# Performance work log

Hardware: AMD Instinct MI355X
Metric: run time of the kernel (lower is better)

## Reference

```python
import jax, jax.numpy as jnp
import numpy as np
from jax import lax

B, N, K, NUM_CLASS = 8, 4096, 16, 13


def knn(pc, k):
    # pc: (B, C, N); returns indices of k nearest neighbors (B, N, k)
    sq = jnp.sum(pc * pc, axis=1)                       # (B, N)
    inner = jnp.einsum('bcn,bcm->bnm', pc, pc)          # (B, N, N)
    neg_dist = 2.0 * inner - sq[:, :, None] - sq[:, None, :]
    return lax.top_k(neg_dist, k)[1]                    # (B, N, k)


def group(fea, idx):
    # fea: (B, C, N), idx: (B, N, k) -> (B, C, N, k)
    return jax.vmap(lambda f, i: f[:, i])(fea, idx)


def mlp2(x, w, b, act=True):
    # 1x1 conv2d: x (B, Cin, N, k) -> (B, Cout, N, k)
    y = jnp.einsum('oc,bcnk->bonk', w, x) + b[None, :, None, None]
    return jax.nn.relu(y) if act else y


def mlp1(x, w, b, act=True):
    # 1x1 conv1d: x (B, Cin, N) -> (B, Cout, N)
    y = jnp.einsum('oc,bcn->bon', w, x) + b[None, :, None]
    return jax.nn.relu(y) if act else y


def edgeconv(xyz, fea, k, wg1, bg1, wg2, bg2, wf1, bf1, wf2, bf2, wf3, bf3):
    idx = knn(fea, k)
    # geometric branch: (B, 10, N, k) = [dist, xyz, xyz_knn, xyz - xyz_knn]
    xk = group(xyz, idx)
    xc = jnp.broadcast_to(xyz[:, :, :, None], xk.shape)
    xr = xc - xk
    xd = jnp.sqrt(jnp.sum(xr * xr, axis=1, keepdims=True))
    g = jnp.concatenate([xd, xc, xk, xr], axis=1)
    # feature branch: (B, 2C, N, k) = [fea, fea_knn]
    fk = group(fea, idx)
    fc = jnp.broadcast_to(fea[:, :, :, None], fk.shape)
    f = jnp.concatenate([fc, fk], axis=1)
    g = mlp2(mlp2(g, wg1, bg1), wg2, bg2)
    f = mlp2(mlp2(mlp2(f, wf1, bf1), wf2, bf2), wf3, bf3)
    return jnp.max(g * f, axis=-1)  # (B, Cout, N)


_SPECS = [
    ('e1_mg1', 10, 32), ('e1_mg2', 32, 32),
    ('e1_mf1', 6, 32), ('e1_mf2', 32, 32), ('e1_mf3', 32, 32),
    ('e2_mg1', 10, 128), ('e2_mg2', 128, 128),
    ('e2_mf1', 64, 128), ('e2_mf2', 128, 128), ('e2_mf3', 128, 128),
    ('c1', 128, 128), ('c2', 128, 1024), ('c3', 1184, 512),
    ('c4', 512, 256), ('c5', 256, 128), ('c6', 128, NUM_CLASS),
]


def setup_inputs() -> dict:
    key = jax.random.key(0)
    ks = jax.random.split(key, 2 * len(_SPECS) + 1)
    inp = {'xyz': jax.random.normal(ks[0], (B, N, 3), dtype=jnp.float32)}
    for j, (name, ci, co) in enumerate(_SPECS):
        scale = 1.0 / np.sqrt(ci)
        inp['w_' + name] = jax.random.normal(ks[2 * j + 1], (co, ci), dtype=jnp.float32) * scale
        inp['b_' + name] = jax.random.normal(ks[2 * j + 2], (co,), dtype=jnp.float32) * 0.01
    return inp


def reference(xyz, w_e1_mg1, b_e1_mg1, w_e1_mg2, b_e1_mg2, w_e1_mf1, b_e1_mf1,
              w_e1_mf2, b_e1_mf2, w_e1_mf3, b_e1_mf3, w_e2_mg1, b_e2_mg1,
              w_e2_mg2, b_e2_mg2, w_e2_mf1, b_e2_mf1, w_e2_mf2, b_e2_mf2,
              w_e2_mf3, b_e2_mf3, w_c1, b_c1, w_c2, b_c2, w_c3, b_c3,
              w_c4, b_c4, w_c5, b_c5, w_c6, b_c6):
    x = jnp.transpose(xyz, (0, 2, 1))  # (B, 3, N)
    fea1 = edgeconv(x, x, K, w_e1_mg1, b_e1_mg1, w_e1_mg2, b_e1_mg2,
                    w_e1_mf1, b_e1_mf1, w_e1_mf2, b_e1_mf2, w_e1_mf3, b_e1_mf3)
    fea2 = edgeconv(x, fea1, K, w_e2_mg1, b_e2_mg1, w_e2_mg2, b_e2_mg2,
                    w_e2_mf1, b_e2_mf1, w_e2_mf2, b_e2_mf2, w_e2_mf3, b_e2_mf3)
    f = mlp1(fea2, w_c1, b_c1)
    f = mlp1(f, w_c2, b_c2)                        # (B, 1024, N)
    g = jnp.max(f, axis=-1, keepdims=True)         # global feature (B, 1024, 1)
    g = jnp.broadcast_to(g, (g.shape[0], g.shape[1], x.shape[2]))
    f = jnp.concatenate([fea1, fea2, g], axis=1)   # (B, 1184, N)
    f = mlp1(f, w_c3, b_c3)
    f = mlp1(f, w_c4, b_c4)
    f = mlp1(f, w_c5, b_c5)
    return mlp1(f, w_c6, b_c6, act=False)          # (B, NUM_CLASS, N)
```

## Files before the change

### kernel.cpp

```cpp
#include <hip/hip_runtime.h>
#include <math.h>

#define B_ 8
#define N_ 4096
#define PL_ (8 * 4096 * 32)

__device__ __forceinline__ unsigned short bf16rne(float x) {
    unsigned int u = __float_as_uint(x);
    return (unsigned short)((u + 0x7FFFu + ((u >> 16) & 1u)) >> 16);
}
__device__ __forceinline__ float bff(unsigned short h) {
    return __uint_as_float((unsigned int)h << 16);
}
__device__ __forceinline__ void cvt_hl(unsigned short* base, int numel, int idx, float x) {
    unsigned short h = bf16rne(x);
    base[idx] = h;
    base[numel + idx] = bf16rne(x - bff(h));
}

typedef __attribute__((ext_vector_type(8))) short bf16x8;
typedef __attribute__((ext_vector_type(4))) float f32x4;

#define MF16(a, b, c) __builtin_amdgcn_mfma_f32_16x16x32_bf16((a), (b), (c), 0, 0, 0)

__global__ __launch_bounds__(256) void prep_kernel(
    const float* __restrict__ w0, const float* __restrict__ w1,
    const float* __restrict__ w2, const float* __restrict__ w3,
    const float* __restrict__ w4, const float* __restrict__ w5,
    const float* __restrict__ w6, const float* __restrict__ w8,
    const float* __restrict__ w9, const float* __restrict__ w10,
    const float* __restrict__ w11, const float* __restrict__ w12,
    const float* __restrict__ w13, const float* __restrict__ w14,
    const float* __restrict__ wf1, const float* __restrict__ bf1,
    const float* __restrict__ xyz,
    float* __restrict__ wt, float* __restrict__ gbuf, float* __restrict__ sqbuf,
    unsigned short* __restrict__ xyzp) {
    const int g = blockIdx.x * 256 + threadIdx.x;
    unsigned short* wus = (unsigned short*)(wt + 3840);

    if (g < 3584) {
        if (g < 320)       { int i = g >> 5, o = g & 31;             wt[g] = w0[o * 10 + i]; }
        else if (g < 1344) { int l = g - 320;  int i = l >> 5, o = l & 31; wt[g] = w1[o * 32 + i]; }
        else if (g < 1536) { int l = g - 1344; int i = l >> 5, o = l & 31; wt[g] = w2[o * 6 + i]; }
        else if (g < 2560) { int l = g - 1536; int i = l >> 5, o = l & 31; wt[g] = w3[o * 32 + i]; }
        else               { int l = g - 2560; int i = l >> 5, o = l & 31; wt[g] = w4[o * 32 + i]; }
    }
    else if (g < 3840)   { int l = g - 3584; wt[g] = (l < 128) ? bf1[l] : 0.0f; }
    else if (g < 12032)  { int l = g - 3840; int o = l >> 5, i = l & 31;
                           float x = (o < 128) ? wf1[o * 64 + i] : wf1[(o - 128) * 64 + 32 + i];
                           cvt_hl(wus + 0, 8192, l, x); }
    else if (g < 28416)  { int l = g - 12032;  cvt_hl(wus + 16384, 16384, l, w10[l]); }
    else if (g < 159488) { int l = g - 28416;  cvt_hl(wus + 49152, 131072, l, w11[l]); }
    else if (g < 241408) { int l = g - 159488; int o = l / 160, i = l - o * 160;
                           cvt_hl(wus + 311296, 81920, l, w12[o * 1184 + i]); }
    else if (g < 372480) { int l = g - 241408; cvt_hl(wus + 475136, 131072, l, w13[l]); }
    else if (g < 405248) { int l = g - 372480; cvt_hl(wus + 737280, 32768, l, w14[l]); }
    else if (g < 409344) { int l = g - 405248; int o = l >> 5, k = l & 31;
                           float x = (k < 10) ? w5[o * 10 + k] : 0.0f;
                           cvt_hl(wus + 802816, 4096, l, x); }
    else if (g < 425728) { int l = g - 409344; cvt_hl(wus + 811008, 16384, l, w6[l]); }
    else if (g < 442112) { int l = g - 425728; cvt_hl(wus + 843776, 16384, l, w8[l]); }
    else if (g < 458496) { int l = g - 442112; cvt_hl(wus + 876544, 16384, l, w9[l]); }
    else if (g < 466688) { gbuf[g - 458496] = 0.0f; }
    else if (g < 499456) { int l = g - 466688;
                           const float* p = xyz + (size_t)l * 3;
                           sqbuf[l] = fmaf(p[0], p[0], fmaf(p[1], p[1], p[2] * p[2])); }
    else if (g < 532224) {
        int row = g - 499456;
        const float* p = xyz + (size_t)row * 3;
        unsigned short hv[8] = {0,0,0,0,0,0,0,0};
        unsigned short mv[8] = {0,0,0,0,0,0,0,0};
        unsigned short lv[8] = {0,0,0,0,0,0,0,0};
        #pragma unroll
        for (int c = 0; c < 3; ++c) {
            float v = p[c];
            unsigned short h = bf16rne(v); float d = v - bff(h);
            unsigned short m = bf16rne(d);
            hv[c] = h; mv[c] = m; lv[c] = bf16rne(d - bff(m));
        }
        uint4 z = make_uint4(0u, 0u, 0u, 0u);
        unsigned short* d0 = xyzp + (size_t)row * 32;
        unsigned short* d1 = d0 + PL_;
        unsigned short* d2 = d0 + 2 * PL_;
        *(uint4*)d0 = *(uint4*)hv; *(uint4*)(d0 + 8) = z; *(uint4*)(d0 + 16) = z; *(uint4*)(d0 + 24) = z;
        *(uint4*)d1 = *(uint4*)mv; *(uint4*)(d1 + 8) = z; *(uint4*)(d1 + 16) = z; *(uint4*)(d1 + 24) = z;
        *(uint4*)d2 = *(uint4*)lv; *(uint4*)(d2 + 8) = z; *(uint4*)(d2 + 16) = z; *(uint4*)(d2 + 24) = z;
    }
}

__global__ __launch_bounds__(256) void fea1p_kernel(
    const float* __restrict__ F, unsigned short* __restrict__ P, float* __restrict__ SQ) {
    int row = blockIdx.x * 256 + threadIdx.x;
    const float* x = F + (size_t)row * 32;
    float s = 0.0f;
    unsigned short hb[32], mb[32], lb[32];
    #pragma unroll
    for (int c = 0; c < 32; ++c) {
        float v = x[c];
        s = fmaf(v, v, s);
        unsigned short h = bf16rne(v); float d = v - bff(h);
        unsigned short m = bf16rne(d);
        hb[c] = h; mb[c] = m; lb[c] = bf16rne(d - bff(m));
    }
    SQ[row] = s;
    unsigned short* d0 = P + (size_t)row * 32;
    #pragma unroll
    for (int q = 0; q < 4; ++q) {
        *(uint4*)(d0 + 8 * q)           = *(uint4*)&hb[8 * q];
        *(uint4*)(d0 + PL_ + 8 * q)     = *(uint4*)&mb[8 * q];
        *(uint4*)(d0 + 2 * PL_ + 8 * q) = *(uint4*)&lb[8 * q];
    }
}


__device__ __forceinline__ void cas_asc(unsigned long long& x, unsigned long long& y) {
    unsigned long long a = x, b = y;
    bool sw = a > b;
    x = sw ? b : a;
    y = sw ? a : b;
}

__device__ __forceinline__ void merge_top(unsigned long long (&k)[16],
                                          const unsigned long long (&o)[16]) {
    #pragma unroll
    for (int i = 0; i < 16; ++i) {
        unsigned long long bb = o[15 - i];
        if (bb > k[i]) k[i] = bb;
    }
    #pragma unroll
    for (int st = 8; st >= 1; st >>= 1)
        #pragma unroll
        for (int i = 0; i < 16; ++i)
            if ((i & st) == 0) cas_asc(k[i], k[i + st]);
}

__device__ __forceinline__ void casv(float& x, float& y) {
    float lo = fminf(x, y), hi = fmaxf(x, y);
    x = lo; y = hi;
}

__device__ __forceinline__ void sortv16(float (&v)[16]) {
    #pragma unroll
    for (int sz = 2; sz <= 16; sz <<= 1)
        #pragma unroll
        for (int st = sz >> 1; st >= 1; st >>= 1)
            #pragma unroll
            for (int i = 0; i < 16; ++i)
                if ((i & st) == 0) {
                    if ((i & sz) == 0) casv(v[i], v[i + st]);
                    else                casv(v[i + st], v[i]);
                }
}

__device__ __forceinline__ void mergev(float (&kv)[16], const float (&nv)[16]) {
    #pragma unroll
    for (int i = 0; i < 16; ++i) kv[i] = fmaxf(kv[i], nv[15 - i]);
    #pragma unroll
    for (int st = 8; st >= 1; st >>= 1)
        #pragma unroll
        for (int i = 0; i < 16; ++i)
            if ((i & st) == 0) casv(kv[i], kv[i + st]);
}

__global__ __launch_bounds__(256, 4) void knn_kernel(
    const unsigned short* __restrict__ P, const float* __restrict__ SQ,
    unsigned long long* __restrict__ Kout) {
    __shared__ __align__(16) char U[64 * 68 * 4];
    __shared__ float sqcL[2048];
    __shared__ float tau[64];
    __shared__ int cnt[64];
    float* Ds = (float*)U;
    unsigned long long* cap = (unsigned long long*)U;
    const int t = threadIdx.x;
    const int b = blockIdx.y;
    const int r0 = blockIdx.x * 64;
    const int half = blockIdx.z;
    const int H0 = half * 2048;
    const int lane = t & 63, w = t >> 6;
    const int lr = lane & 15, lg = lane >> 4;
    const int kb = lg << 3;
    const int sr = t & 63, sq = t >> 6;
    const int pw = lg ^ (w & 3);
    const int psr = ((sr >> 2) ^ (sr >> 4)) & 3;

    for (int i = t; i < 2048; i += 256) sqcL[i] = SQ[(size_t)b * N_ + H0 + i];

    const unsigned short* ap = P + ((size_t)(b * N_) + r0 + 16 * w + lr) * 32 + kb;
    const bf16x8 ah = *(const bf16x8*)ap;
    const bf16x8 am = *(const bf16x8*)(ap + PL_);
    const bf16x8 al = *(const bf16x8*)(ap + 2 * PL_);
    const f32x4 sqr4 = *(const f32x4*)&SQ[(size_t)b * N_ + r0 + 16 * w + 4 * lg];

    float kv[16];
    #pragma unroll
    for (int j = 0; j < 16; ++j) kv[j] = -3.4e38f;

    __syncthreads();

    for (int c0 = H0; c0 < H0 + 2048; c0 += 64) {
        #pragma unroll
        for (int j = 0; j < 4; ++j) {
            const unsigned short* bp = P + ((size_t)(b * N_) + c0 + 16 * j + lr) * 32 + kb;
            bf16x8 bh = *(const bf16x8*)bp;
            bf16x8 bm = *(const bf16x8*)(bp + PL_);
            bf16x8 bl = *(const bf16x8*)(bp + 2 * PL_);
            f32x4 a = {0.0f, 0.0f, 0.0f, 0.0f};
            a = MF16(ah, bh, a); a = MF16(am, bh, a); a = MF16(ah, bm, a);
            a = MF16(am, bm, a); a = MF16(al, bh, a); a = MF16(ah, bl, a);
            float sqcv = sqcL[c0 - H0 + 16 * j + lr];
            int colsw = 16 * j + ((((lr >> 2) ^ pw) & 3) << 2) + (lr & 3);
            #pragma unroll
            for (int r = 0; r < 4; ++r) {
                float e = fmaf(2.0f, a[r], -sqr4[r]) - sqcv;
                Ds[(16 * w + 4 * lg + r) * 68 + colsw] = e;
            }
        }
        __syncthreads();
        float nv[16];
        #pragma unroll
        for (int q = 0; q < 4; ++q)
            *(float4*)&nv[4 * q] = *(const float4*)&Ds[sr * 68 + sq * 16 + (((q ^ psr) & 3) << 2)];
        sortv16(nv);
        mergev(kv, nv);
        __syncthreads();
    }

    float* QLf = (float*)U;
    #pragma unroll
    for (int j = 0; j < 16; ++j) QLf[sr * 68 + sq * 16 + j] = kv[j];
    __syncthreads();
    if (t < 64) {
        float K[16];
        #pragma unroll
        for (int j = 0; j < 16; ++j) K[j] = QLf[t * 68 + j];
        #pragma unroll
        for (int q = 1; q < 4; ++q) {
            float Tt[16];
            #pragma unroll
            for (int j = 0; j < 16; ++j) Tt[j] = QLf[t * 68 + q * 16 + j];
            #pragma unroll
            for (int i = 0; i < 16; ++i) K[i] = fmaxf(K[i], Tt[15 - i]);
            #pragma unroll
            for (int st = 8; st >= 1; st >>= 1)
                #pragma unroll
                for (int i = 0; i < 16; ++i)
                    if ((i & st) == 0) casv(K[i], K[i + st]);
        }
        tau[t] = K[0];
        cnt[t] = 0;
    }
    __syncthreads();
    const f32x4 taur4 = *(const f32x4*)&tau[16 * w + 4 * lg];

    for (int c0 = H0; c0 < H0 + 2048; c0 += 64) {
        #pragma unroll
        for (int j = 0; j < 4; ++j) {
            const unsigned short* bp = P + ((size_t)(b * N_) + c0 + 16 * j + lr) * 32 + kb;
            bf16x8 bh = *(const bf16x8*)bp;
            bf16x8 bm = *(const bf16x8*)(bp + PL_);
            bf16x8 bl = *(const bf16x8*)(bp + 2 * PL_);
            f32x4 a = {0.0f, 0.0f, 0.0f, 0.0f};
            a = MF16(ah, bh, a); a = MF16(am, bh, a); a = MF16(ah, bm, a);
            a = MF16(am, bm, a); a = MF16(al, bh, a); a = MF16(ah, bl, a);
            float sqcv = sqcL[c0 - H0 + 16 * j + lr];
            #pragma unroll
            for (int r = 0; r < 4; ++r) {
                float e = fmaf(2.0f, a[r], -sqr4[r]) - sqcv;
                if (e >= taur4[r]) {
                    int row = 16 * w + 4 * lg + r;
                    unsigned int u = __float_as_uint(e);
                    unsigned int ou = (u & 0x80000000u) ? ~u : (u | 0x80000000u);
                    unsigned long long key = ((unsigned long long)ou << 32)
                                           | (unsigned int)(4095 - (c0 + 16 * j + lr));
                    int pos = atomicAdd(&cnt[row], 1);
                    if (pos < 32) cap[row * 32 + pos] = key;
                }
            }
        }
    }
    __syncthreads();

    if (t < 64) {
        int n = min(cnt[t], 32);
        unsigned long long K[16];
        #pragma unroll
        for (int j = 0; j < 16; ++j) K[j] = 0ull;
        for (int i = 0; i < n; ++i) {
            unsigned long long v = cap[t * 32 + i];
            if (v > K[0]) {
                K[0] = v;
                #pragma unroll
                for (int s = 0; s < 15; ++s) cas_asc(K[s], K[s + 1]);
            }
        }
        size_t obase = (((size_t)b * 2 + half) * N_ + r0 + t) * 16;
        #pragma unroll
        for (int j = 0; j < 16; ++j) Kout[obase + j] = K[j];
    }
}

__global__ __launch_bounds__(256) void knn_merge_kernel(
    const unsigned long long* __restrict__ Kbuf, int* __restrict__ IDX) {
    int gid = blockIdx.x * 256 + threadIdx.x;
    int b = gid >> 12, r = gid & 4095;
    unsigned long long K0[16], K1[16];
    const unsigned long long* p0 = Kbuf + (((size_t)b * 2 + 0) * N_ + r) * 16;
    const unsigned long long* p1 = Kbuf + (((size_t)b * 2 + 1) * N_ + r) * 16;
    #pragma unroll
    for (int j = 0; j < 16; ++j) { K0[j] = p0[j]; K1[j] = p1[j]; }
    merge_top(K0, K1);
    size_t ob = ((size_t)b * N_ + r) * 16;
    #pragma unroll
    for (int j = 0; j < 16; ++j)
        IDX[ob + j] = 4095 - (int)(unsigned int)(K0[15 - j] & 0xFFFFFFFFu);
}


__global__ __launch_bounds__(256, 4) void e1_kernel(
    const float* __restrict__ xyz, const int* __restrict__ idx1,
    const float* __restrict__ wte1,
    const float* __restrict__ bg1, const float* __restrict__ bg2,
    const float* __restrict__ bf1, const float* __restrict__ bf2,
    const float* __restrict__ bf3,
    float* __restrict__ fea1) {
    __shared__ __align__(16) float Ain[10 * 132];
    __shared__ __align__(16) float Bu0[32 * 132];
    __shared__ __align__(16) float Bu1[32 * 132];
    __shared__ __align__(16) float wl[3584];
    __shared__ float bl[5][32];
    __shared__ __align__(16) float Pm1[4][8][32];
    __shared__ int idxl[128];
    const int t = threadIdx.x;
    const int b = blockIdx.x >> 9;
    const int n0 = (blockIdx.x & 511) << 3;
    const int et = (t & 31) << 2;
    const int ct = (t >> 5) << 2;

    for (int i = t; i < 3584; i += 256) wl[i] = wte1[i];
    if (t < 32) {
        bl[0][t] = bg1[t]; bl[1][t] = bg2[t]; bl[2][t] = bf1[t];
        bl[3][t] = bf2[t]; bl[4][t] = bf3[t];
    }
    if (t < 128) idxl[t] = idx1[((size_t)b * N_ + n0 + (t >> 4)) * 16 + (t & 15)];
    __syncthreads();
    if (t < 128) {
        int p = t >> 4, n = n0 + p, m = idxl[t];
        const float* xc = xyz + ((size_t)b * N_ + n) * 3;
        const float* xk = xyz + ((size_t)b * N_ + m) * 3;
        float c0 = xc[0], c1v = xc[1], c2v = xc[2];
        float k0 = xk[0], k1 = xk[1], k2 = xk[2];
        float r0 = c0 - k0, r1 = c1v - k1, r2 = c2v - k2;
        Ain[0 * 132 + t] = sqrtf(r0 * r0 + r1 * r1 + r2 * r2);
        Ain[1 * 132 + t] = c0;  Ain[2 * 132 + t] = c1v; Ain[3 * 132 + t] = c2v;
        Ain[4 * 132 + t] = k0;  Ain[5 * 132 + t] = k1;  Ain[6 * 132 + t] = k2;
        Ain[7 * 132 + t] = r0;  Ain[8 * 132 + t] = r1;  Ain[9 * 132 + t] = r2;
    }
    __syncthreads();

    float acc[4][4];
    auto gem = [&](int KK, const float* Asrc, int woff) {
        #pragma unroll
        for (int ii = 0; ii < 4; ++ii)
            #pragma unroll
            for (int jj = 0; jj < 4; ++jj) acc[ii][jj] = 0.0f;
        for (int i = 0; i < KK; ++i) {
            float a4[4], w4[4];
            *(float4*)a4 = *(const float4*)&Asrc[i * 132 + et];
            *(float4*)w4 = *(const float4*)&wl[woff + i * 32 + ct];
            #pragma unroll
            for (int ii = 0; ii < 4; ++ii)
                #pragma unroll
                for (int jj = 0; jj < 4; ++jj)
                    acc[ii][jj] = fmaf(a4[ii], w4[jj], acc[ii][jj]);
        }
    };
    auto wrout = [&](float* dst, const float* brow) {
        #pragma unroll
        for (int jj = 0; jj < 4; ++jj) {
            float tmp[4];
            #pragma unroll
            for (int ii = 0; ii < 4; ++ii) tmp[ii] = fmaxf(acc[ii][jj] + brow[ct + jj], 0.0f);
            *(float4*)&dst[(ct + jj) * 132 + et] = *(float4*)tmp;
        }
    };

    gem(10, Ain, 0);          wrout(Bu1, bl[0]);   __syncthreads();
    gem(32, Bu1, 320);
    float g2r[4][4];
    #pragma unroll
    for (int ii = 0; ii < 4; ++ii)
        #pragma unroll
        for (int jj = 0; jj < 4; ++jj)
            g2r[ii][jj] = fmaxf(acc[ii][jj] + bl[1][ct + jj], 0.0f);
    gem(6, Ain + 132, 1344);  wrout(Bu0, bl[2]);   __syncthreads();
    gem(32, Bu0, 1536);       wrout(Bu1, bl[3]);   __syncthreads();
    gem(32, Bu1, 2560);

    float pm[4];
    #pragma unroll
    for (int jj = 0; jj < 4; ++jj) {
        float mx = 0.0f;
        #pragma unroll
        for (int ii = 0; ii < 4; ++ii) {
            float f3 = fmaxf(acc[ii][jj] + bl[4][ct + jj], 0.0f);
            mx = fmaxf(mx, g2r[ii][jj] * f3);
        }
        pm[jj] = mx;
    }
    const int sub = t & 3, pl = (t & 31) >> 2;
    *(float4*)&Pm1[sub][pl][ct] = *(float4*)pm;
    __syncthreads();
    {
        int p = t >> 5, c = t & 31;
        float v = fmaxf(fmaxf(Pm1[0][p][c], Pm1[1][p][c]), fmaxf(Pm1[2][p][c], Pm1[3][p][c]));
        fea1[((size_t)b * N_ + n0 + p) * 32 + c] = v;
    }
}


__global__ __launch_bounds__(256, 2) void e2_kernel(
    const float* __restrict__ xyz, const int* __restrict__ idx2,
    const float* __restrict__ CfPf,
    const unsigned short* __restrict__ wg1p, const unsigned short* __restrict__ wg2p,
    const unsigned short* __restrict__ wf2p, const unsigned short* __restrict__ wf3p,
    const float* __restrict__ bg1, const float* __restrict__ bg2,
    const float* __restrict__ bf2, const float* __restrict__ bf3,
    float* __restrict__ fea2) {
    __shared__ __align__(16) unsigned short Ah[128 * 128];
    __shared__ __align__(16) unsigned short Al[128 * 128];
    __shared__ float bb[4][128];
    __shared__ int idxl[128];
    const int t = threadIdx.x;
    const int b = blockIdx.x >> 9;
    const int n0 = (blockIdx.x & 511) << 3;
    const int lane = t & 63, w = t >> 6;
    const int wr = (w >> 1) << 6;
    const int wc = (w & 1) << 6;
    const int lr = lane & 15, lg = lane >> 4;
    const int kb = lg << 3;

    auto swz = [](int e, int bo) { return e * 256 + (bo ^ ((e & 7) << 4)); };

    for (int i = t; i < 512; i += 256) {
        const float* bp = (i < 128) ? bg1 : (i < 256) ? bg2 : (i < 384) ? bf2 : bf3;
        bb[i >> 7][i & 127] = bp[i & 127];
    }
    if (t < 128) idxl[t] = idx2[((size_t)b * N_ + n0 + (t >> 4)) * 16 + (t & 15)];
    __syncthreads();

    f32x4 acc[4][4];
    const f32x4 zz = {0.0f, 0.0f, 0.0f, 0.0f};
    auto zacc = [&]() {
        #pragma unroll
        for (int i = 0; i < 4; ++i)
            #pragma unroll
            for (int j = 0; j < 4; ++j) acc[i][j] = zz;
    };

    {
        bf16x8 gbh[4], gbl[4];
        #pragma unroll
        for (int j = 0; j < 4; ++j) {
            float gv[8];
            #pragma unroll
            for (int q = 0; q < 8; ++q) gv[q] = 0.0f;
            if (lg < 2) {
                int e = wc + j * 16 + lr;
                int p = e >> 4, m = idxl[e];
                const float* xc = xyz + ((size_t)b * N_ + n0 + p) * 3;
                const float* xk = xyz + ((size_t)b * N_ + m) * 3;
                float c0 = xc[0], c1 = xc[1], c2 = xc[2];
                float k0 = xk[0], k1 = xk[1], k2 = xk[2];
                float r0 = c0 - k0, r1 = c1 - k1, r2 = c2 - k2;
                if (lg == 0) {
                    gv[0] = sqrtf(r0 * r0 + r1 * r1 + r2 * r2);
                    gv[1] = c0; gv[2] = c1; gv[3] = c2;
                    gv[4] = k0; gv[5] = k1; gv[6] = k2; gv[7] = r0;
                } else { gv[0] = r1; gv[1] = r2; }
            }
            bf16x8 vh, vl;
            #pragma unroll
            for (int q = 0; q < 8; ++q) {
                unsigned short h = bf16rne(gv[q]);
                vh[q] = (short)h;
                vl[q] = (short)bf16rne(gv[q] - bff(h));
            }
            gbh[j] = vh; gbl[j] = vl;
        }
        zacc();
        #pragma unroll
        for (int i = 0; i < 4; ++i) {
            size_t off = (size_t)(wr + i * 16 + lr) * 32 + kb;
            bf16x8 wh = *(const bf16x8*)(wg1p + off);
            bf16x8 wl_ = *(const bf16x8*)(wg1p + 4096 + off);
            #pragma unroll
            for (int j = 0; j < 4; ++j) {
                acc[i][j] = MF16(wh, gbh[j], acc[i][j]);
                acc[i][j] = MF16(wl_, gbh[j], acc[i][j]);
                acc[i][j] = MF16(wh, gbl[j], acc[i][j]);
            }
        }
    }

    auto epi_store = [&](const float* brow) {
        #pragma unroll
        for (int i = 0; i < 4; ++i) {
            int o4 = wr + i * 16 + lg * 4;
            float bv[4];
            *(float4*)bv = *(const float4*)&brow[o4];
            #pragma unroll
            for (int j = 0; j < 4; ++j) {
                int e = wc + j * 16 + lr;
                unsigned short h[4], l[4];
                #pragma unroll
                for (int r = 0; r < 4; ++r) {
                    float v = fmaxf(acc[i][j][r] + bv[r], 0.0f);
                    h[r] = bf16rne(v);
                    l[r] = bf16rne(v - bff(h[r]));
                }
                int bo = swz(e, o4 * 2);
                *(ushort4*)((char*)Ah + bo) = make_ushort4(h[0], h[1], h[2], h[3]);
                *(ushort4*)((char*)Al + bo) = make_ushort4(l[0], l[1], l[2], l[3]);
            }
        }
    };
    epi_store(bb[0]);
    __syncthreads();

    auto gemmK = [&](const unsigned short* __restrict__ Wp) {
        zacc();
        #pragma unroll
        for (int ks = 0; ks < 4; ++ks) {
            bf16x8 xh[4], xl[4];
            #pragma unroll
            for (int j = 0; j < 4; ++j) {
                int e = wc + j * 16 + lr;
                int bo = swz(e, (ks * 32 + kb) * 2);
                xh[j] = *(const bf16x8*)((const char*)Ah + bo);
                xl[j] = *(const bf16x8*)((const char*)Al + bo);
            }
            #pragma unroll
            for (int i = 0; i < 4; ++i) {
                size_t off = (size_t)(wr + i * 16 + lr) * 128 + ks * 32 + kb;
                bf16x8 wh = *(const bf16x8*)(Wp + off);
                bf16x8 wl_ = *(const bf16x8*)(Wp + 16384 + off);
                #pragma unroll
                for (int j = 0; j < 4; ++j) {
                    acc[i][j] = MF16(wh, xh[j], acc[i][j]);
                    acc[i][j] = MF16(wl_, xh[j], acc[i][j]);
                    acc[i][j] = MF16(wh, xl[j], acc[i][j]);
                }
            }
        }
    };

    gemmK(wg2p);
    float g2r[4][4][4];
    #pragma unroll
    for (int i = 0; i < 4; ++i) {
        float bv[4];
        *(float4*)bv = *(const float4*)&bb[1][wr + i * 16 + lg * 4];
        #pragma unroll
        for (int j = 0; j < 4; ++j)
            #pragma unroll
            for (int r = 0; r < 4; ++r)
                g2r[i][j][r] = fmaxf(acc[i][j][r] + bv[r], 0.0f);
    }
    __syncthreads();

    {
        int e = t & 127, hf = t >> 7;
        int n = n0 + (e >> 4), m = idxl[e];
        const float* crow = CfPf + ((size_t)b * N_ + n) * 256 + hf * 64;
        const float* prow = CfPf + ((size_t)b * N_ + m) * 256 + 128 + hf * 64;
        #pragma unroll
        for (int q = 0; q < 16; ++q) {
            float4 cc = *(const float4*)(crow + q * 4);
            float4 pp = *(const float4*)(prow + q * 4);
            float v[4] = { fmaxf(cc.x + pp.x, 0.0f), fmaxf(cc.y + pp.y, 0.0f),
                           fmaxf(cc.z + pp.z, 0.0f), fmaxf(cc.w + pp.w, 0.0f) };
            unsigned short h[4], l[4];
            #pragma unroll
            for (int r = 0; r < 4; ++r) {
                h[r] = bf16rne(v[r]);
                l[r] = bf16rne(v[r] - bff(h[r]));
            }
            int bo = swz(e, (hf * 64 + q * 4) * 2);
            *(ushort4*)((char*)Ah + bo) = make_ushort4(h[0], h[1], h[2], h[3]);
            *(ushort4*)((char*)Al + bo) = make_ushort4(l[0], l[1], l[2], l[3]);
        }
    }
    __syncthreads();

    gemmK(wf2p);
    __syncthreads();
    epi_store(bb[2]);
    __syncthreads();

    gemmK(wf3p);
    #pragma unroll
    for (int j = 0; j < 4; ++j) {
        int p = (wc >> 4) + j;
        #pragma unroll
        for (int i = 0; i < 4; ++i) {
            int o4 = wr + i * 16 + lg * 4;
            float bv[4];
            *(float4*)bv = *(const float4*)&bb[3][o4];
            float vr[4];
            #pragma unroll
            for (int r = 0; r < 4; ++r) {
                float f3v = fmaxf(acc[i][j][r] + bv[r], 0.0f);
                float v = g2r[i][j][r] * f3v;
                v = fmaxf(v, __shfl_xor(v, 1));
                v = fmaxf(v, __shfl_xor(v, 2));
                v = fmaxf(v, __shfl_xor(v, 4));
                v = fmaxf(v, __shfl_xor(v, 8));
                vr[r] = v;
            }
            if (lr == 0)
                *(float4*)(fea2 + ((size_t)b * N_ + n0 + p) * 128 + o4) = *(float4*)vr;
        }
    }
}


template<int RELU, int BMODE, int GMAX>
__global__ __launch_bounds__(256) void gemm_mfma(
    const float* __restrict__ X1, int S1, int K1,
    const float* __restrict__ X2, int S2, int Ktot,
    const unsigned short* __restrict__ Wc, const float* __restrict__ bias,
    float* __restrict__ Y, int COUT, float* __restrict__ gout) {
    __shared__ __align__(16) unsigned short Xh[128 * 40];
    __shared__ __align__(16) unsigned short Xl[128 * 40];
    __shared__ __align__(16) unsigned short Wh[128 * 40];
    __shared__ __align__(16) unsigned short Wl[128 * 40];
    __shared__ float Gm[2][128];
    const int t = threadIdx.x;
    const int m0 = blockIdx.x * 128, o0 = blockIdx.y * 128;
    const int lane = t & 63, w = t >> 6;
    const int wr = (w >> 1) << 6, wc = (w & 1) << 6;
    const int lr = lane & 15, lg = lane >> 4;
    const int kb = lg << 3;
    const size_t WN = (size_t)COUT * Ktot;

    f32x4 acc[4][4];
    const f32x4 zz = {0.0f, 0.0f, 0.0f, 0.0f};
    #pragma unroll
    for (int i = 0; i < 4; ++i)
        #pragma unroll
        for (int j = 0; j < 4; ++j) acc[i][j] = zz;

    const int ntile = Ktot >> 5;
    for (int kt = 0; kt < ntile; ++kt) {
        const int kbase = kt << 5;
        const float* Xp; int S, koff;
        if (kbase < K1) { Xp = X1; S = S1; koff = kbase; }
        else            { Xp = X2; S = S2; koff = kbase - K1; }
        #pragma unroll
        for (int rr = 0; rr < 4; ++rr) {
            int idx = t + rr * 256;
            int p = idx >> 3, i4 = (idx & 7) << 2;
            const float4 v = *(const float4*)(Xp + (size_t)(m0 + p) * S + koff + i4);
            unsigned short h0 = bf16rne(v.x), h1 = bf16rne(v.y);
            unsigned short h2 = bf16rne(v.z), h3 = bf16rne(v.w);
            *(ushort4*)&Xh[p * 40 + i4] = make_ushort4(h0, h1, h2, h3);
            *(ushort4*)&Xl[p * 40 + i4] = make_ushort4(
                bf16rne(v.x - bff(h0)), bf16rne(v.y - bff(h1)),
                bf16rne(v.z - bff(h2)), bf16rne(v.w - bff(h3)));
        }
        #pragma unroll
        for (int rr = 0; rr < 2; ++rr) {
            int c = t + rr * 256;
            int o = c >> 2, k8 = (c & 3) << 3;
            const unsigned short* src = Wc + (size_t)(o0 + o) * Ktot + kbase + k8;
            *(uint4*)&Wh[o * 40 + k8] = *(const uint4*)src;
            *(uint4*)&Wl[o * 40 + k8] = *(const uint4*)(src + WN);
        }
        __syncthreads();

        bf16x8 ah[4], al[4], bh[4], bl[4];
        #pragma unroll
        for (int f = 0; f < 4; ++f) {
            ah[f] = *(const bf16x8*)&Xh[(wr + f * 16 + lr) * 40 + kb];
            al[f] = *(const bf16x8*)&Xl[(wr + f * 16 + lr) * 40 + kb];
            bh[f] = *(const bf16x8*)&Wh[(wc + f * 16 + lr) * 40 + kb];
            bl[f] = *(const bf16x8*)&Wl[(wc + f * 16 + lr) * 40 + kb];
        }
        #pragma unroll
        for (int i = 0; i < 4; ++i)
            #pragma unroll
            for (int j = 0; j < 4; ++j) {
                acc[i][j] = MF16(ah[i], bh[j], acc[i][j]);
                acc[i][j] = MF16(al[i], bh[j], acc[i][j]);
                acc[i][j] = MF16(ah[i], bl[j], acc[i][j]);
            }
        __syncthreads();
    }

    const int b = m0 >> 12;
    if (GMAX) {
        #pragma unroll
        for (int j = 0; j < 4; ++j) {
            const int oc = wc + j * 16 + lr;
            const float bv = bias[o0 + oc];
            float mx = 0.0f;
            #pragma unroll
            for (int i = 0; i < 4; ++i)
                #pragma unroll
                for (int r = 0; r < 4; ++r) {
                    float v = acc[i][j][r] + bv;
                    if (RELU) v = fmaxf(v, 0.0f);
                    mx = fmaxf(mx, v);
                }
            mx = fmaxf(mx, __shfl_xor(mx, 16));
            mx = fmaxf(mx, __shfl_xor(mx, 32));
            if (lane < 16) Gm[w >> 1][wc + j * 16 + lane] = mx;
        }
        __syncthreads();
        if (t < 128) {
            float v = fmaxf(Gm[0][t], Gm[1][t]);
            atomicMax((unsigned int*)(gout + b * 1024 + o0 + t), __float_as_uint(v));
        }
    } else {
        #pragma unroll
        for (int j = 0; j < 4; ++j) {
            const int oc = wc + j * 16 + lr;
            const float bv = (BMODE == 0) ? bias[o0 + oc] : bias[b * 512 + o0 + oc];
            #pragma unroll
            for (int i = 0; i < 4; ++i) {
                float* yp = Y + (size_t)(m0 + wr + i * 16 + lg * 4) * COUT + o0 + oc;
                #pragma unroll
                for (int r = 0; r < 4; ++r) {
                    float v = acc[i][j][r] + bv;
                    if (RELU) v = fmaxf(v, 0.0f);
                    yp[(size_t)r * COUT] = v;
                }
            }
        }
    }
}


__global__ void bias3_kernel(const float* __restrict__ g, const float* __restrict__ w_c3,
                             const float* __restrict__ b_c3, float* __restrict__ bias3) {
    __shared__ float gs[1024];
    int b = blockIdx.x >> 1;
    int o = ((blockIdx.x & 1) << 8) + threadIdx.x;
    for (int i = threadIdx.x; i < 1024; i += 256) gs[i] = g[b * 1024 + i];
    __syncthreads();
    float acc = b_c3[o];
    const float* wr = w_c3 + (size_t)o * 1184 + 160;
    for (int i = 0; i < 1024; i += 4) {
        float4 w4 = *(const float4*)(wr + i);
        acc = fmaf(w4.x, gs[i], acc);     acc = fmaf(w4.y, gs[i + 1], acc);
        acc = fmaf(w4.z, gs[i + 2], acc); acc = fmaf(w4.w, gs[i + 3], acc);
    }
    bias3[b * 512 + o] = acc;
}


__global__ __launch_bounds__(256, 1) void c6_kernel(
    const float* __restrict__ h5, const float* __restrict__ w,
    const float* __restrict__ bias, float* __restrict__ out) {
    __shared__ float ws[13 * 128];
    __shared__ float bs[13];
    int t = threadIdx.x;
    for (int i = t; i < 13 * 128; i += 256) ws[i] = w[i];
    if (t < 13) bs[t] = bias[t];
    __syncthreads();
    int b = blockIdx.x >> 4;
    int n = ((blockIdx.x & 15) << 8) + t;
    float x[128];
    const float* xp = h5 + ((size_t)b * N_ + n) * 128;
    #pragma unroll
    for (int i = 0; i < 128; i += 4) *(float4*)&x[i] = *(const float4*)(xp + i);
    for (int o = 0; o < 13; ++o) {
        float acc = bs[o];
        #pragma unroll
        for (int i = 0; i < 128; ++i) acc = fmaf(ws[o * 128 + i], x[i], acc);
        out[((size_t)b * 13 + o) * N_ + n] = acc;
    }
}


extern "C" void kernel_launch(void* const* d_in, const int* in_sizes, int n_in,
                              void* d_out, int out_size, void* d_ws, size_t ws_size,
                              hipStream_t stream) {
    (void)in_sizes; (void)n_in; (void)out_size; (void)ws_size;
    const float* xyz = (const float*)d_in[0];
    #define W_(j)  ((const float*)d_in[1 + 2 * (j)])
    #define Bp_(j) ((const float*)d_in[2 + 2 * (j)])

    char* ws = (char*)d_ws;
    const size_t MB = 1u << 20;
    int*   idx1  = (int*)(ws + 0 * MB);
    int*   idx2  = (int*)(ws + 2 * MB);
    float* fea1  = (float*)(ws + 4 * MB);
    float* CfPf  = (float*)(ws + 8 * MB);
    float* fea2  = (float*)(ws + 40 * MB);
    float* h1    = (float*)(ws + 56 * MB);
    float* sqbuf = (float*)(ws + 72 * MB);
    float* gbuf  = (float*)(ws + 72 * MB + (128u << 10));
    float* b3buf = (float*)(ws + 72 * MB + (160u << 10));
    float* wt    = (float*)(ws + 72 * MB + (176u << 10));
    float* h3    = (float*)(ws + 75 * MB);
    float* h4    = CfPf;
    float* h5    = h1;
    float* outp  = (float*)d_out;
    unsigned long long* Kbuf = (unsigned long long*)(ws + 75 * MB);
    unsigned short* xyzp = (unsigned short*)(ws + 8 * MB);
    unsigned short* feap = (unsigned short*)(ws + 14 * MB);

    float* wte1  = wt;
    float* bpre  = wt + 3584;
    const unsigned short* wus = (const unsigned short*)(wt + 3840);
    const unsigned short* wpre = wus + 0;
    const unsigned short* wc1  = wus + 16384;
    const unsigned short* wc2  = wus + 49152;
    const unsigned short* wc3  = wus + 311296;
    const unsigned short* wc4  = wus + 475136;
    const unsigned short* wc5  = wus + 737280;
    const unsigned short* wg1p = wus + 802816;
    const unsigned short* wg2p = wus + 811008;
    const unsigned short* wf2p = wus + 843776;
    const unsigned short* wf3p = wus + 876544;

    prep_kernel<<<2079, 256, 0, stream>>>(
        W_(0), W_(1), W_(2), W_(3), W_(4), W_(5), W_(6), W_(8), W_(9), W_(10),
        W_(11), W_(12), W_(13), W_(14), W_(7), Bp_(7), xyz, wt, gbuf, sqbuf, xyzp);

    knn_kernel<<<dim3(64, 8, 2), 256, 0, stream>>>(xyzp, sqbuf, Kbuf);
    knn_merge_kernel<<<128, 256, 0, stream>>>(Kbuf, idx1);
    e1_kernel<<<4096, 256, 0, stream>>>(xyz, idx1, wte1, Bp_(0), Bp_(1), Bp_(2), Bp_(3), Bp_(4), fea1);

    fea1p_kernel<<<128, 256, 0, stream>>>(fea1, feap, sqbuf);
    knn_kernel<<<dim3(64, 8, 2), 256, 0, stream>>>(feap, sqbuf, Kbuf);
    knn_merge_kernel<<<128, 256, 0, stream>>>(Kbuf, idx2);
    gemm_mfma<0, 0, 0><<<dim3(256, 2), 256, 0, stream>>>(fea1, 32, 32, nullptr, 0, 32,
                                                         wpre, bpre, CfPf, 256, nullptr);
    e2_kernel<<<4096, 256, 0, stream>>>(xyz, idx2, CfPf, wg1p, wg2p, wf2p, wf3p,
                                        Bp_(5), Bp_(6), Bp_(8), Bp_(9), fea2);

    gemm_mfma<1, 0, 0><<<dim3(256, 1), 256, 0, stream>>>(fea2, 128, 128, nullptr, 0, 128,
                                                         wc1, Bp_(10), h1, 128, nullptr);
    gemm_mfma<1, 0, 1><<<dim3(256, 8), 256, 0, stream>>>(h1, 128, 128, nullptr, 0, 128,
                                                         wc2, Bp_(11), nullptr, 1024, gbuf);
    bias3_kernel<<<16, 256, 0, stream>>>(gbuf, W_(12), Bp_(12), b3buf);
    gemm_mfma<1, 1, 0><<<dim3(256, 4), 256, 0, stream>>>(fea1, 32, 32, fea2, 128, 160,
                                                         wc3, b3buf, h3, 512, nullptr);
    gemm_mfma<1, 0, 0><<<dim3(256, 2), 256, 0, stream>>>(h3, 512, 512, nullptr, 0, 512,
                                                         wc4, Bp_(13), h4, 256, nullptr);
    gemm_mfma<1, 0, 0><<<dim3(256, 1), 256, 0, stream>>>(h4, 256, 256, nullptr, 0, 256,
                                                         wc5, Bp_(14), h5, 128, nullptr);
    c6_kernel<<<128, 256, 0, stream>>>(h5, W_(15), Bp_(15), outp);
    #undef W_
    #undef Bp_
}
```

Baseline: 1.162 ms.

## Stage KNN candidate tiles in LDS and do per-wave top-k merge via shuffles

The KNN kernel now loads each 64-column candidate tile (hi/mid/lo bf16 planes) once into shared memory for the whole block. Previously each of the four waves fetched it separately from global memory. The distance tile is now per-wave, so each wave sorts its own 16 rows, dropping a block-wide barrier per tile. The final per-row top-k merge across lanes uses xor shuffles instead of an LDS round trip. Squared norms are read from global instead of an LDS copy. In exchange there are two barriers per tile for the staging, and the code relies on wave-level LDS ordering without explicit syncs.

After: 1.119 ms. -3.7%, faster.

```diff
diff --git a/kernel.cpp b/kernel.cpp
--- a/kernel.cpp
+++ b/kernel.cpp
@@ -165,12 +165,10 @@
 __global__ __launch_bounds__(256, 4) void knn_kernel(
     const unsigned short* __restrict__ P, const float* __restrict__ SQ,
     unsigned long long* __restrict__ Kout) {
-    __shared__ __align__(16) char U[64 * 68 * 4];
-    __shared__ float sqcL[2048];
-    __shared__ float tau[64];
+    __shared__ __align__(16) unsigned short Bs[3][64][40];
+    __shared__ __align__(16) char U[17408];
+    __shared__ float tau_sm[64];
     __shared__ int cnt[64];
-    float* Ds = (float*)U;
-    unsigned long long* cap = (unsigned long long*)U;
     const int t = threadIdx.x;
     const int b = blockIdx.y;
     const int r0 = blockIdx.x * 64;
@@ -179,11 +177,10 @@
     const int lane = t & 63, w = t >> 6;
     const int lr = lane & 15, lg = lane >> 4;
     const int kb = lg << 3;
-    const int sr = t & 63, sq = t >> 6;
-    const int pw = lg ^ (w & 3);
-    const int psr = ((sr >> 2) ^ (sr >> 4)) & 3;
-
-    for (int i = t; i < 2048; i += 256) sqcL[i] = SQ[(size_t)b * N_ + H0 + i];
+    const int sc = t >> 2, sq8 = (t & 3) << 3;
+
+    float* Ds = (float*)U + w * 1088;
+    unsigned long long* cap = (unsigned long long*)U;
 
     const unsigned short* ap = P + ((size_t)(b * N_) + r0 + 16 * w + lr) * 32 + kb;
     const bf16x8 ah = *(const bf16x8*)ap;
@@ -191,78 +188,79 @@
     const bf16x8 al = *(const bf16x8*)(ap + 2 * PL_);
     const f32x4 sqr4 = *(const f32x4*)&SQ[(size_t)b * N_ + r0 + 16 * w + 4 * lg];
 
+    const float* SQc = SQ + (size_t)b * N_ + H0;
+    const unsigned short* Pc = P + ((size_t)(b * N_) + H0) * 32;
+
     float kv[16];
     #pragma unroll
     for (int j = 0; j < 16; ++j) kv[j] = -3.4e38f;
 
-    __syncthreads();
-
-    for (int c0 = H0; c0 < H0 + 2048; c0 += 64) {
+    for (int tt = 0; tt < 32; ++tt) {
+        __syncthreads();
+        {
+            const unsigned short* src = Pc + (size_t)(tt * 64 + sc) * 32 + sq8;
+            *(uint4*)&Bs[0][sc][sq8] = *(const uint4*)src;
+            *(uint4*)&Bs[1][sc][sq8] = *(const uint4*)(src + PL_);
+            *(uint4*)&Bs[2][sc][sq8] = *(const uint4*)(src + 2 * PL_);
+        }
+        __syncthreads();
         #pragma unroll
         for (int j = 0; j < 4; ++j) {
-            const unsigned short* bp = P + ((size_t)(b * N_) + c0 + 16 * j + lr) * 32 + kb;
-            bf16x8 bh = *(const bf16x8*)bp;
-            bf16x8 bm = *(const bf16x8*)(bp + PL_);
-            bf16x8 bl = *(const bf16x8*)(bp + 2 * PL_);
+            int cc = 16 * j + lr;
+            bf16x8 bh = *(const bf16x8*)&Bs[0][cc][kb];
+            bf16x8 bm = *(const bf16x8*)&Bs[1][cc][kb];
+            bf16x8 bl = *(const bf16x8*)&Bs[2][cc][kb];
             f32x4 a = {0.0f, 0.0f, 0.0f, 0.0f};
             a = MF16(ah, bh, a); a = MF16(am, bh, a); a = MF16(ah, bm, a);
             a = MF16(am, bm, a); a = MF16(al, bh, a); a = MF16(ah, bl, a);
-            float sqcv = sqcL[c0 - H0 + 16 * j + lr];
-            int colsw = 16 * j + ((((lr >> 2) ^ pw) & 3) << 2) + (lr & 3);
-            #pragma unroll
-            for (int r = 0; r < 4; ++r) {
-                float e = fmaf(2.0f, a[r], -sqr4[r]) - sqcv;
-                Ds[(16 * w + 4 * lg + r) * 68 + colsw] = e;
-            }
-        }
-        __syncthreads();
+            float sqcv = SQc[tt * 64 + cc];
+            #pragma unroll
+            for (int r = 0; r < 4; ++r)
+                Ds[(4 * lg + r) * 68 + cc] = fmaf(2.0f, a[r], -sqr4[r]) - sqcv;
+        }
         float nv[16];
         #pragma unroll
         for (int q = 0; q < 4; ++q)
-            *(float4*)&nv[4 * q] = *(const float4*)&Ds[sr * 68 + sq * 16 + (((q ^ psr) & 3) << 2)];
+            *(float4*)&nv[4 * q] = *(const float4*)&Ds[lr * 68 + lg * 16 + 4 * q];
         sortv16(nv);
         mergev(kv, nv);
+    }
+
+    #pragma unroll
+    for (int st = 16; st <= 32; st <<= 1) {
+        float ov[16];
+        #pragma unroll
+        for (int i = 0; i < 16; ++i) ov[i] = __shfl_xor(kv[15 - i], st);
+        #pragma unroll
+        for (int i = 0; i < 16; ++i) kv[i] = fmaxf(kv[i], ov[i]);
+        #pragma unroll
+        for (int s2 = 8; s2 >= 1; s2 >>= 1)
+            #pragma unroll
+            for (int i = 0; i < 16; ++i)
+                if ((i & s2) == 0) casv(kv[i], kv[i + s2]);
+    }
+    if (lane < 16) { tau_sm[w * 16 + lane] = kv[0]; cnt[w * 16 + lane] = 0; }
+    const f32x4 taur4 = *(const f32x4*)&tau_sm[w * 16 + 4 * lg];
+
+    for (int tt = 0; tt < 32; ++tt) {
         __syncthreads();
-    }
-
-    float* QLf = (float*)U;
-    #pragma unroll
-    for (int j = 0; j < 16; ++j) QLf[sr * 68 + sq * 16 + j] = kv[j];
-    __syncthreads();
-    if (t < 64) {
-        float K[16];
-        #pragma unroll
-        for (int j = 0; j < 16; ++j) K[j] = QLf[t * 68 + j];
-        #pragma unroll
-        for (int q = 1; q < 4; ++q) {
-            float Tt[16];
-            #pragma unroll
-            for (int j = 0; j < 16; ++j) Tt[j] = QLf[t * 68 + q * 16 + j];
-            #pragma unroll
-            for (int i = 0; i < 16; ++i) K[i] = fmaxf(K[i], Tt[15 - i]);
-            #pragma unroll
-            for (int st = 8; st >= 1; st >>= 1)
-                #pragma unroll
-                for (int i = 0; i < 16; ++i)
-                    if ((i & st) == 0) casv(K[i], K[i + st]);
-        }
-        tau[t] = K[0];
-        cnt[t] = 0;
-    }
-    __syncthreads();
-    const f32x4 taur4 = *(const f32x4*)&tau[16 * w + 4 * lg];
-
-    for (int c0 = H0; c0 < H0 + 2048; c0 += 64) {
+        {
+            const unsigned short* src = Pc + (size_t)(tt * 64 + sc) * 32 + sq8;
+            *(uint4*)&Bs[0][sc][sq8] = *(const uint4*)src;
+            *(uint4*)&Bs[1][sc][sq8] = *(const uint4*)(src + PL_);
+            *(uint4*)&Bs[2][sc][sq8] = *(const uint4*)(src + 2 * PL_);
+        }
+        __syncthreads();
         #pragma unroll
         for (int j = 0; j < 4; ++j) {
-            const unsigned short* bp = P + ((size_t)(b * N_) + c0 + 16 * j + lr) * 32 + kb;
-            bf16x8 bh = *(const bf16x8*)bp;
-            bf16x8 bm = *(const bf16x8*)(bp + PL_);
-            bf16x8 bl = *(const bf16x8*)(bp + 2 * PL_);
+            int cc = 16 * j + lr;
+            bf16x8 bh = *(const bf16x8*)&Bs[0][cc][kb];
+            bf16x8 bm = *(const bf16x8*)&Bs[1][cc][kb];
+            bf16x8 bl = *(const bf16x8*)&Bs[2][cc][kb];
             f32x4 a = {0.0f, 0.0f, 0.0f, 0.0f};
             a = MF16(ah, bh, a); a = MF16(am, bh, a); a = MF16(ah, bm, a);
             a = MF16(am, bm, a); a = MF16(al, bh, a); a = MF16(ah, bl, a);
-            float sqcv = sqcL[c0 - H0 + 16 * j + lr];
+            float sqcv = SQc[tt * 64 + cc];
             #pragma unroll
             for (int r = 0; r < 4; ++r) {
                 float e = fmaf(2.0f, a[r], -sqr4[r]) - sqcv;
@@ -271,7 +269,7 @@
                     unsigned int u = __float_as_uint(e);
                     unsigned int ou = (u & 0x80000000u) ? ~u : (u | 0x80000000u);
                     unsigned long long key = ((unsigned long long)ou << 32)
-                                           | (unsigned int)(4095 - (c0 + 16 * j + lr));
+                                           | (unsigned int)(4095 - (H0 + tt * 64 + cc));
                     int pos = atomicAdd(&cnt[row], 1);
                     if (pos < 32) cap[row * 32 + pos] = key;
                 }
```
